# Kernel tuning notes

Measured on AMD Instinct MI355X. Metric: run time of the kernel, lower is better.

The kernel has to match this reference:

```python
import jax, jax.numpy as jnp
import numpy as np

N = 50000          # nodes
E = 1_600_000      # edges (avg degree 32)
H = 2              # attention heads per layer
F = 64             # per-head feature dim
NC = 16            # num_classes
NEG_SLOPE = 0.2    # PyG GATConv default leaky relu slope


def setup_inputs():
    key = jax.random.key(0)
    ks = jax.random.split(key, 20)
    s = 0.05
    z = jnp.zeros
    inp = {
        'x': jax.random.normal(ks[0], (N, 64), dtype=jnp.float32),
        'edge_index': jax.random.randint(ks[1], (2, E), 0, N, dtype=jnp.int32),
        # GAT layer 1: in=64 (heads=1 concat from input), out=H*F
        'W1': jax.random.normal(ks[2], (64, H * F)) * s,
        'a_src1': jax.random.normal(ks[3], (H, F)) * s,
        'a_dst1': jax.random.normal(ks[4], (H, F)) * s,
        'b1': z((H * F,)),
        # GAT layer 2: in=H*F=128, out=H*F
        'W2': jax.random.normal(ks[5], (H * F, H * F)) * s,
        'a_src2': jax.random.normal(ks[6], (H, F)) * s,
        'a_dst2': jax.random.normal(ks[7], (H, F)) * s,
        'b2': z((H * F,)),
        # MLP head: 128 -> 512 -> 256 -> NC
        'lw1': jax.random.normal(ks[8], (H * F, 512)) * s, 'lb1': z((512,)),
        'lw2': jax.random.normal(ks[9], (512, 256)) * s, 'lb2': z((256,)),
        'lw3': jax.random.normal(ks[10], (256, NC)) * s, 'lb3': z((NC,)),
    }
    return inp


def gat_conv(x, src, dst, W, a_src, a_dst, b):
    """PyG-style GATConv (shared weights for src/dst), head concat output."""
    h = (x @ W).reshape(-1, H, F)                       # [N, H, F]
    alpha_s = jnp.einsum('nhf,hf->nh', h, a_src)        # [N, H]
    alpha_d = jnp.einsum('nhf,hf->nh', h, a_dst)
    e = jax.nn.leaky_relu(alpha_s[src] + alpha_d[dst], NEG_SLOPE)  # [E', H]
    # segment softmax over incoming edges of each dst node
    e_max = jax.ops.segment_max(e, dst, num_segments=N)            # [N, H]
    e_exp = jnp.exp(e - e_max[dst])
    denom = jax.ops.segment_sum(e_exp, dst, num_segments=N)
    alpha = e_exp / (denom[dst] + 1e-16)                            # [E', H]
    msg = h[src] * alpha[:, :, None]                                # [E', H, F]
    out = jax.ops.segment_sum(msg, dst, num_segments=N)             # [N, H, F]
    return out.reshape(N, H * F) + b


def reference(x, edge_index, W1, a_src1, a_dst1, b1, W2, a_src2, a_dst2, b2,
              lw1, lb1, lw2, lb2, lw3, lb3):
    # add self loops (PyG GATConv default)
    loop = jnp.arange(N, dtype=edge_index.dtype)
    src = jnp.concatenate([edge_index[0], loop])
    dst = jnp.concatenate([edge_index[1], loop])

    h = jax.nn.relu(gat_conv(x, src, dst, W1, a_src1, a_dst1, b1))
    emb = jax.nn.relu(gat_conv(h, src, dst, W2, a_src2, a_dst2, b2))

    z = jax.nn.relu(emb @ lw1 + lb1)
    z = jax.nn.relu(z @ lw2 + lb2)
    logits = z @ lw3 + lb3
    return emb, logits
```

## Files before the change

kernel.cpp:

```cpp
#include <hip/hip_runtime.h>

typedef __bf16 bf16f __attribute__((ext_vector_type(8)));
typedef float  f32x4 __attribute__((ext_vector_type(4)));

__device__ __forceinline__ float bf2f(unsigned short u) {
  union { unsigned int u; float f; } v;
  v.u = ((unsigned int)u) << 16;
  return v.f;
}
__device__ __forceinline__ unsigned short f2bf(float f) {
  union { float f; unsigned int u; } v; v.f = f;
  unsigned int r = v.u + 0x7FFFu + ((v.u >> 16) & 1u);
  return (unsigned short)(r >> 16);
}
__device__ __forceinline__ float bflo(unsigned int w) {
  union { unsigned int u; float f; } v; v.u = w << 16; return v.f;
}
__device__ __forceinline__ float bfhi(unsigned int w) {
  union { unsigned int u; float f; } v; v.u = w & 0xFFFF0000u; return v.f;
}

__global__ void GNNModel_general_12077448036407_kernel(int* cnt, int ncnt) {
  int i = blockIdx.x * blockDim.x + threadIdx.x;
  if (i < ncnt) cnt[i] = 0;
}

__global__ void wpack2_kernel(const float* __restrict__ lw1, unsigned short* __restrict__ Wb1,
                              const float* __restrict__ lw2, unsigned short* __restrict__ Wb2) {
  int i = blockIdx.x * blockDim.x + threadIdx.x;
  if (i < 512 * 128) {
    int n = i >> 7, k = i & 127;
    Wb1[i] = f2bf(lw1[(size_t)k * 512 + n]);
  }
  if (i < 256 * 512) {
    int n = i >> 9, k = i & 511;
    Wb2[i] = f2bf(lw2[(size_t)k * 256 + n]);
  }
}

__launch_bounds__(256)
__global__ void gr_fused_kernel(const float* __restrict__ x, const float* __restrict__ W1,
                                unsigned short* __restrict__ hb, int M, int gblocks,
                                const int* __restrict__ dst, int* __restrict__ cnt,
                                unsigned short* __restrict__ rank, int E) {
  __shared__ float As[16][132];
  __shared__ float Bs[16][136];
  int bid = blockIdx.x;
  int t = threadIdx.x;

  if (bid >= gblocks) {
    int e = (bid - gblocks) * 256 + t;
    if (e < E) {
      int r = atomicAdd(&cnt[dst[e]], 1);
      rank[e] = (unsigned short)r;
    }
    return;
  }

  int tx = t & 15, ty = t >> 4;
  int m0 = bid * 128;

  float acc[8][8];
#pragma unroll
  for (int i = 0; i < 8; i++)
#pragma unroll
    for (int j = 0; j < 8; j++) acc[i][j] = 0.0f;

  int arow = t >> 1;
  int akc  = (t & 1) * 8;
  int bkk  = t >> 4;
  int bnn  = (t & 15) * 8;
  int gm = m0 + arow;

  for (int k0 = 0; k0 < 64; k0 += 16) {
    float av[8];
    if (gm < M) {
      const float* Af = x + (size_t)gm * 64 + k0 + akc;
      float4 r0 = *(const float4*)Af;
      float4 r1 = *(const float4*)(Af + 4);
      av[0] = r0.x; av[1] = r0.y; av[2] = r0.z; av[3] = r0.w;
      av[4] = r1.x; av[5] = r1.y; av[6] = r1.z; av[7] = r1.w;
    } else {
#pragma unroll
      for (int j = 0; j < 8; j++) av[j] = 0.0f;
    }
#pragma unroll
    for (int j = 0; j < 8; j++) As[akc + j][arow] = av[j];

    const float* bp = W1 + (size_t)(k0 + bkk) * 128 + bnn;
    float4 b0 = *(const float4*)bp;
    float4 b1 = *(const float4*)(bp + 4);
    *(float4*)&Bs[bkk][bnn]     = b0;
    *(float4*)&Bs[bkk][bnn + 4] = b1;

    __syncthreads();

#pragma unroll 4
    for (int kk = 0; kk < 16; kk++) {
      float a[8], b[8];
      *(float4*)&a[0] = *(const float4*)&As[kk][ty * 8];
      *(float4*)&a[4] = *(const float4*)&As[kk][ty * 8 + 4];
      *(float4*)&b[0] = *(const float4*)&Bs[kk][tx * 8];
      *(float4*)&b[4] = *(const float4*)&Bs[kk][tx * 8 + 4];
#pragma unroll
      for (int i = 0; i < 8; i++)
#pragma unroll
        for (int j = 0; j < 8; j++)
          acc[i][j] = fmaf(a[i], b[j], acc[i][j]);
    }
    __syncthreads();
  }

#pragma unroll
  for (int i = 0; i < 8; i++) {
    int m = m0 + ty * 8 + i;
    if (m >= M) continue;
    unsigned short* Cp = hb + (size_t)m * 128 + tx * 8;
    uint4 pk;
    pk.x = (unsigned int)f2bf(acc[i][0]) | ((unsigned int)f2bf(acc[i][1]) << 16);
    pk.y = (unsigned int)f2bf(acc[i][2]) | ((unsigned int)f2bf(acc[i][3]) << 16);
    pk.z = (unsigned int)f2bf(acc[i][4]) | ((unsigned int)f2bf(acc[i][5]) << 16);
    pk.w = (unsigned int)f2bf(acc[i][6]) | ((unsigned int)f2bf(acc[i][7]) << 16);
    *(uint4*)Cp = pk;
  }
}

__global__ void scan1_kernel(const int* __restrict__ cnt, int* __restrict__ offs,
                             int* __restrict__ bsum, int M) {
  __shared__ int sh[256];
  int t = threadIdx.x;
  int i = blockIdx.x * 256 + t;
  int v = (i < M) ? cnt[i] : 0;
  sh[t] = v;
  __syncthreads();
  for (int off = 1; off < 256; off <<= 1) {
    int u = (t >= off) ? sh[t - off] : 0;
    __syncthreads();
    sh[t] += u;
    __syncthreads();
  }
  if (i <= M) offs[i] = sh[t] - v;
  if (t == 255) bsum[blockIdx.x] = sh[255];
}

__global__ void scan2_kernel(int* __restrict__ bsum, int NB) {
  __shared__ int sh[256];
  int t = threadIdx.x;
  int v = (t < NB) ? bsum[t] : 0;
  sh[t] = v;
  __syncthreads();
  for (int off = 1; off < 256; off <<= 1) {
    int u = (t >= off) ? sh[t - off] : 0;
    __syncthreads();
    sh[t] += u;
    __syncthreads();
  }
  if (t < NB) bsum[t] = sh[t] - v;
}

__global__ void scan3_kernel(int* __restrict__ offs, const int* __restrict__ bsum, int M) {
  int i = blockIdx.x * 256 + threadIdx.x;
  if (i <= M) offs[i] += bsum[i >> 8];
}

__global__ void pa_fused_kernel(const unsigned short* __restrict__ hb,
                                const float* __restrict__ a_src,
                                const float* __restrict__ a_dst,
                                float2* __restrict__ aSp, float2* __restrict__ aDp,
                                int M, int ablocks,
                                const int* __restrict__ src, const int* __restrict__ dstp,
                                const unsigned short* __restrict__ rank,
                                const int* __restrict__ offs, int* __restrict__ csr, int E) {
  int bid = blockIdx.x;
  int t = threadIdx.x;

  if (bid >= ablocks) {
    int e = (bid - ablocks) * 256 + t;
    if (e < E) {
      int p = offs[dstp[e]] + (int)rank[e];
      __builtin_nontemporal_store(src[e], &csr[p]);
    }
    return;
  }

  int gw = (bid * 256 + t) >> 6;
  int lane = t & 63;
  if (gw >= M) return;
  float h0 = bf2f(hb[(size_t)gw * 128 + lane]);
  float h1 = bf2f(hb[(size_t)gw * 128 + 64 + lane]);
  float as0 = h0 * a_src[lane];
  float as1 = h1 * a_src[64 + lane];
  float ad0 = h0 * a_dst[lane];
  float ad1 = h1 * a_dst[64 + lane];
  for (int o = 32; o; o >>= 1) {
    as0 += __shfl_xor(as0, o);
    as1 += __shfl_xor(as1, o);
    ad0 += __shfl_xor(ad0, o);
    ad1 += __shfl_xor(ad1, o);
  }
  if (lane == 0) {
    aSp[gw] = make_float2(as0, as1);
    aDp[gw] = make_float2(ad0, ad1);
  }
}

__launch_bounds__(256)
__global__ void m128_kernel(const void* __restrict__ A,
                            const unsigned short* __restrict__ Bw,
                            const float* __restrict__ bias, void* __restrict__ C,
                            int M, int K, int Nt, int aBF, int cBF, int relu) {
  __shared__ unsigned short As[128 * 32];
  __shared__ unsigned short Bs[128 * 32];
  int tid = threadIdx.x;
  int wid = tid >> 6, lane = tid & 63;
  int lm = lane & 15, quad = lane >> 4;
  int wr = wid >> 1, wc = wid & 1;
  int n0 = blockIdx.x * 128, m0 = blockIdx.y * 128;

  f32x4 acc[4][4];
#pragma unroll
  for (int mi = 0; mi < 4; mi++)
#pragma unroll
    for (int ni = 0; ni < 4; ni++)
#pragma unroll
      for (int i = 0; i < 4; i++) acc[mi][ni][i] = 0.0f;

  int c0 = (wid << 6) + lane;
  int c1 = c0 + 256;
  int srow = tid >> 1;
  int skc  = (tid & 1) << 4;

  for (int k0 = 0; k0 < K; k0 += 32) {
    {
      const unsigned short* g0 = Bw + (size_t)(n0 + (c0 >> 2)) * K + k0 + ((c0 & 3) << 3);
      __builtin_amdgcn_global_load_lds((const __attribute__((address_space(1))) void*)g0,
                                       (__attribute__((address_space(3))) void*)(Bs + (wid << 9)),
                                       16, 0, 0);
      const unsigned short* g1 = Bw + (size_t)(n0 + (c1 >> 2)) * K + k0 + ((c1 & 3) << 3);
      __builtin_amdgcn_global_load_lds((const __attribute__((address_space(1))) void*)g1,
                                       (__attribute__((address_space(3))) void*)(Bs + 2048 + (wid << 9)),
                                       16, 0, 0);
    }
    if (aBF) {
      int r0 = m0 + (c0 >> 2); if (r0 > M - 1) r0 = M - 1;
      const unsigned short* g0 = (const unsigned short*)A + (size_t)r0 * K + k0 + ((c0 & 3) << 3);
      __builtin_amdgcn_global_load_lds((const __attribute__((address_space(1))) void*)g0,
                                       (__attribute__((address_space(3))) void*)(As + (wid << 9)),
                                       16, 0, 0);
      int r1 = m0 + (c1 >> 2); if (r1 > M - 1) r1 = M - 1;
      const unsigned short* g1 = (const unsigned short*)A + (size_t)r1 * K + k0 + ((c1 & 3) << 3);
      __builtin_amdgcn_global_load_lds((const __attribute__((address_space(1))) void*)g1,
                                       (__attribute__((address_space(3))) void*)(As + 2048 + (wid << 9)),
                                       16, 0, 0);
    } else {
      int gm = m0 + srow;
      uint4 p0, p1;
      if (gm < M) {
        const float* Af = (const float*)A + (size_t)gm * K + k0 + skc;
        float4 r0 = *(const float4*)Af;
        float4 r1 = *(const float4*)(Af + 4);
        float4 r2 = *(const float4*)(Af + 8);
        float4 r3 = *(const float4*)(Af + 12);
        p0.x = (unsigned int)f2bf(r0.x) | ((unsigned int)f2bf(r0.y) << 16);
        p0.y = (unsigned int)f2bf(r0.z) | ((unsigned int)f2bf(r0.w) << 16);
        p0.z = (unsigned int)f2bf(r1.x) | ((unsigned int)f2bf(r1.y) << 16);
        p0.w = (unsigned int)f2bf(r1.z) | ((unsigned int)f2bf(r1.w) << 16);
        p1.x = (unsigned int)f2bf(r2.x) | ((unsigned int)f2bf(r2.y) << 16);
        p1.y = (unsigned int)f2bf(r2.z) | ((unsigned int)f2bf(r2.w) << 16);
        p1.z = (unsigned int)f2bf(r3.x) | ((unsigned int)f2bf(r3.y) << 16);
        p1.w = (unsigned int)f2bf(r3.z) | ((unsigned int)f2bf(r3.w) << 16);
      } else {
        p0.x = p0.y = p0.z = p0.w = 0u;
        p1.x = p1.y = p1.z = p1.w = 0u;
      }
      *(uint4*)&As[srow * 32 + skc] = p0;
      *(uint4*)&As[srow * 32 + skc + 8] = p1;
    }
    __syncthreads();

    bf16f afr[4], bfr[4];
#pragma unroll
    for (int mi = 0; mi < 4; mi++)
      afr[mi] = *(const bf16f*)&As[(wr * 64 + mi * 16 + lm) * 32 + quad * 8];
#pragma unroll
    for (int ni = 0; ni < 4; ni++)
      bfr[ni] = *(const bf16f*)&Bs[(wc * 64 + ni * 16 + lm) * 32 + quad * 8];
#pragma unroll
    for (int mi = 0; mi < 4; mi++)
#pragma unroll
      for (int ni = 0; ni < 4; ni++)
        acc[mi][ni] = __builtin_amdgcn_mfma_f32_16x16x32_bf16(afr[mi], bfr[ni], acc[mi][ni], 0, 0, 0);
    __syncthreads();
  }

#pragma unroll
  for (int ni = 0; ni < 4; ni++) {
    int col = n0 + wc * 64 + ni * 16 + lm;
    float bv = (bias != 0) ? bias[col] : 0.0f;
#pragma unroll
    for (int mi = 0; mi < 4; mi++) {
#pragma unroll
      for (int i = 0; i < 4; i++) {
        int row = m0 + wr * 64 + mi * 16 + quad * 4 + i;
        if (row < M) {
          float v = acc[mi][ni][i] + bv;
          if (relu) v = fmaxf(v, 0.0f);
          if (cBF) ((unsigned short*)C)[(size_t)row * Nt + col] = f2bf(v);
          else     ((float*)C)[(size_t)row * Nt + col] = v;
        }
      }
    }
  }
}

__launch_bounds__(256)
__global__ void lgemm_kernel(const unsigned short* __restrict__ A,
                             const float* __restrict__ W,
                             const float* __restrict__ bias, float* __restrict__ C,
                             int M, int K) {
  __shared__ unsigned short Bt[16 * 264];
  int tid = threadIdx.x;
  int wave = tid >> 6, lane = tid & 63;
  int lm = lane & 15, quad = lane >> 4;
  int m0 = blockIdx.x * 64;

  for (int f0 = tid * 4; f0 < K * 16; f0 += 1024) {
    float4 w4 = *(const float4*)(W + f0);
    int k = f0 >> 4, n = f0 & 15;
    Bt[(n + 0) * 264 + k] = f2bf(w4.x);
    Bt[(n + 1) * 264 + k] = f2bf(w4.y);
    Bt[(n + 2) * 264 + k] = f2bf(w4.z);
    Bt[(n + 3) * 264 + k] = f2bf(w4.w);
  }
  __syncthreads();

  f32x4 acc;
#pragma unroll
  for (int i = 0; i < 4; i++) acc[i] = 0.0f;

  int m = m0 + wave * 16 + lm;
  const unsigned short* Ap = A + (size_t)m * K;

  for (int k0 = 0; k0 < K; k0 += 32) {
    bf16f af;
#pragma unroll
    for (int j = 0; j < 8; j++) af[j] = (__bf16)0.0f;
    if (m < M) af = *(const bf16f*)(Ap + k0 + quad * 8);
    bf16f bfv = *(const bf16f*)&Bt[lm * 264 + k0 + quad * 8];
    acc = __builtin_amdgcn_mfma_f32_16x16x32_bf16(af, bfv, acc, 0, 0, 0);
  }

  float bv = bias[lm];
#pragma unroll
  for (int i = 0; i < 4; i++) {
    int row = m0 + wave * 16 + quad * 4 + i;
    if (row < M) C[(size_t)row * 16 + lm] = acc[i] + bv;
  }
}

__launch_bounds__(256)
__global__ void tgemm_kernel(const void* __restrict__ A, const float* __restrict__ W,
                             const float* __restrict__ bias, void* __restrict__ C,
                             int M, int K, int Nt, int aBF, int cBF, int relu) {
  __shared__ float As[16][132];
  __shared__ float Bs[16][136];
  int t = threadIdx.x;
  int tx = t & 15, ty = t >> 4;
  int m0 = blockIdx.x * 128, n0 = blockIdx.y * 128;

  float acc[8][8];
#pragma unroll
  for (int i = 0; i < 8; i++)
#pragma unroll
    for (int j = 0; j < 8; j++) acc[i][j] = 0.0f;

  int arow = t >> 1;
  int akc  = (t & 1) * 8;
  int bkk  = t >> 4;
  int bnn  = (t & 15) * 8;
  int gm = m0 + arow;

  for (int k0 = 0; k0 < K; k0 += 16) {
    float av[8];
    if (gm < M) {
      if (aBF) {
        const unsigned short* Ab = (const unsigned short*)A + (size_t)gm * K + k0 + akc;
        uint4 raw = *(const uint4*)Ab;
        av[0] = bflo(raw.x); av[1] = bfhi(raw.x);
        av[2] = bflo(raw.y); av[3] = bfhi(raw.y);
        av[4] = bflo(raw.z); av[5] = bfhi(raw.z);
        av[6] = bflo(raw.w); av[7] = bfhi(raw.w);
      } else {
        const float* Af = (const float*)A + (size_t)gm * K + k0 + akc;
        float4 r0 = *(const float4*)Af;
        float4 r1 = *(const float4*)(Af + 4);
        av[0] = r0.x; av[1] = r0.y; av[2] = r0.z; av[3] = r0.w;
        av[4] = r1.x; av[5] = r1.y; av[6] = r1.z; av[7] = r1.w;
      }
    } else {
#pragma unroll
      for (int j = 0; j < 8; j++) av[j] = 0.0f;
    }
#pragma unroll
    for (int j = 0; j < 8; j++) As[akc + j][arow] = av[j];

    const float* bp = W + (size_t)(k0 + bkk) * Nt + n0 + bnn;
    float4 b0 = *(const float4*)bp;
    float4 b1 = *(const float4*)(bp + 4);
    *(float4*)&Bs[bkk][bnn]     = b0;
    *(float4*)&Bs[bkk][bnn + 4] = b1;

    __syncthreads();

#pragma unroll 4
    for (int kk = 0; kk < 16; kk++) {
      float a[8], b[8];
      *(float4*)&a[0] = *(const float4*)&As[kk][ty * 8];
      *(float4*)&a[4] = *(const float4*)&As[kk][ty * 8 + 4];
      *(float4*)&b[0] = *(const float4*)&Bs[kk][tx * 8];
      *(float4*)&b[4] = *(const float4*)&Bs[kk][tx * 8 + 4];
#pragma unroll
      for (int i = 0; i < 8; i++)
#pragma unroll
        for (int j = 0; j < 8; j++)
          acc[i][j] = fmaf(a[i], b[j], acc[i][j]);
    }
    __syncthreads();
  }

  float bv[8];
#pragma unroll
  for (int j = 0; j < 8; j++) bv[j] = (bias != 0) ? bias[n0 + tx * 8 + j] : 0.0f;

#pragma unroll
  for (int i = 0; i < 8; i++) {
    int m = m0 + ty * 8 + i;
    if (m >= M) continue;
    float v[8];
#pragma unroll
    for (int j = 0; j < 8; j++) {
      float s = acc[i][j] + bv[j];
      v[j] = relu ? fmaxf(s, 0.0f) : s;
    }
    if (cBF) {
      unsigned short* Cp = (unsigned short*)C + (size_t)m * Nt + n0 + tx * 8;
      uint4 pk;
      pk.x = (unsigned int)f2bf(v[0]) | ((unsigned int)f2bf(v[1]) << 16);
      pk.y = (unsigned int)f2bf(v[2]) | ((unsigned int)f2bf(v[3]) << 16);
      pk.z = (unsigned int)f2bf(v[4]) | ((unsigned int)f2bf(v[5]) << 16);
      pk.w = (unsigned int)f2bf(v[6]) | ((unsigned int)f2bf(v[7]) << 16);
      *(uint4*)Cp = pk;
    } else {
      float* Cp = (float*)C + (size_t)m * Nt + n0 + tx * 8;
      float4 o0; o0.x = v[0]; o0.y = v[1]; o0.z = v[2]; o0.w = v[3];
      float4 o1; o1.x = v[4]; o1.y = v[5]; o1.z = v[6]; o1.w = v[7];
      *(float4*)Cp = o0;
      *(float4*)(Cp + 4) = o1;
    }
  }
}

__global__ void alphas_kernel(const unsigned short* __restrict__ hb,
                              const float* __restrict__ a_src,
                              const float* __restrict__ a_dst,
                              float2* __restrict__ aSp, float2* __restrict__ aDp, int M) {
  int gw = (blockIdx.x * blockDim.x + threadIdx.x) >> 6;
  int lane = threadIdx.x & 63;
  if (gw >= M) return;
  float h0 = bf2f(hb[(size_t)gw * 128 + lane]);
  float h1 = bf2f(hb[(size_t)gw * 128 + 64 + lane]);
  float as0 = h0 * a_src[lane];
  float as1 = h1 * a_src[64 + lane];
  float ad0 = h0 * a_dst[lane];
  float ad1 = h1 * a_dst[64 + lane];
  for (int o = 32; o; o >>= 1) {
    as0 += __shfl_xor(as0, o);
    as1 += __shfl_xor(as1, o);
    ad0 += __shfl_xor(ad0, o);
    ad1 += __shfl_xor(ad1, o);
  }
  if (lane == 0) {
    aSp[gw] = make_float2(as0, as1);
    aDp[gw] = make_float2(ad0, ad1);
  }
}

__global__ void aggregate_kernel(const unsigned short* __restrict__ hb,
                                 const float2* __restrict__ aSp,
                                 const float2* __restrict__ aDp,
                                 const int* __restrict__ csr_src, const int* __restrict__ offs,
                                 const float* __restrict__ bias,
                                 float* __restrict__ out, int M) {
  int n = (blockIdx.x * blockDim.x + threadIdx.x) >> 6;
  int lane = threadIdx.x & 63;
  if (n >= M) return;
  int g = lane >> 4;
  int q = lane & 15;
  int h0sel = (q < 8);

  float2 adn = aDp[n];
  float2 asn = aSp[n];
  float e0 = asn.x + adn.x; e0 = (e0 > 0.0f) ? e0 : 0.2f * e0;
  float e1 = asn.y + adn.y; e1 = (e1 > 0.0f) ? e1 : 0.2f * e1;
  float ws0 = expf(e0), ws1 = expf(e1);
  float wself = h0sel ? ws0 : ws1;

  float acc[8];
  if (g == 0) {
    uint4 rv = *(const uint4*)(hb + (size_t)n * 128 + q * 8);
    acc[0] = wself * bflo(rv.x); acc[1] = wself * bfhi(rv.x);
    acc[2] = wself * bflo(rv.y); acc[3] = wself * bfhi(rv.y);
    acc[4] = wself * bflo(rv.z); acc[5] = wself * bfhi(rv.z);
    acc[6] = wself * bflo(rv.w); acc[7] = wself * bfhi(rv.w);
  } else {
#pragma unroll
    for (int i = 0; i < 8; i++) acc[i] = 0.0f;
  }

  float lp0 = 0.0f, lp1 = 0.0f;
  int rs = offs[n], re = offs[n + 1];
  for (int base = rs; base < re; base += 64) {
    int cnt = re - base; if (cnt > 64) cnt = 64;
    int s = 0; float w0 = 0.0f, w1 = 0.0f;
    if (lane < cnt) {
      s = csr_src[base + lane];
      float2 a = aSp[s];
      float f0 = a.x + adn.x; f0 = (f0 > 0.0f) ? f0 : 0.2f * f0;
      float f1 = a.y + adn.y; f1 = (f1 > 0.0f) ? f1 : 0.2f * f1;
      w0 = expf(f0); w1 = expf(f1);
      lp0 += w0; lp1 += w1;
    }
    int jmax = (cnt + 3) >> 2;
#pragma unroll 2
    for (int j = 0; j < jmax; j++) {
      int el = 4 * j + g;
      int sj  = __shfl(s, el);
      float w0j = __shfl(w0, el);
      float w1j = __shfl(w1, el);
      float wj = h0sel ? w0j : w1j;
      uint4 rv = *(const uint4*)(hb + (size_t)sj * 128 + q * 8);
      acc[0] = fmaf(wj, bflo(rv.x), acc[0]);
      acc[1] = fmaf(wj, bfhi(rv.x), acc[1]);
      acc[2] = fmaf(wj, bflo(rv.y), acc[2]);
      acc[3] = fmaf(wj, bfhi(rv.y), acc[3]);
      acc[4] = fmaf(wj, bflo(rv.z), acc[4]);
      acc[5] = fmaf(wj, bfhi(rv.z), acc[5]);
      acc[6] = fmaf(wj, bflo(rv.w), acc[6]);
      acc[7] = fmaf(wj, bfhi(rv.w), acc[7]);
    }
  }
#pragma unroll
  for (int i = 0; i < 8; i++) {
    acc[i] += __shfl_xor(acc[i], 16);
    acc[i] += __shfl_xor(acc[i], 32);
  }
  for (int o = 32; o; o >>= 1) {
    lp0 += __shfl_xor(lp0, o);
    lp1 += __shfl_xor(lp1, o);
  }
  if (g == 0) {
    float linv = 1.0f / ((h0sel ? lp0 + ws0 : lp1 + ws1) + 1e-16f);
    const float* bp = bias + q * 8;
    float4 o0, o1;
    o0.x = fmaxf(acc[0] * linv + bp[0], 0.0f);
    o0.y = fmaxf(acc[1] * linv + bp[1], 0.0f);
    o0.z = fmaxf(acc[2] * linv + bp[2], 0.0f);
    o0.w = fmaxf(acc[3] * linv + bp[3], 0.0f);
    o1.x = fmaxf(acc[4] * linv + bp[4], 0.0f);
    o1.y = fmaxf(acc[5] * linv + bp[5], 0.0f);
    o1.z = fmaxf(acc[6] * linv + bp[6], 0.0f);
    o1.w = fmaxf(acc[7] * linv + bp[7], 0.0f);
    float* op = out + (size_t)n * 128 + q * 8;
    *(float4*)op = o0;
    *(float4*)(op + 4) = o1;
  }
}

extern "C" void kernel_launch(void* const* d_in, const int* in_sizes, int n_in,
                              void* d_out, int out_size, void* d_ws, size_t ws_size,
                              hipStream_t stream) {
  const int N = in_sizes[0] / 64;
  const int E = in_sizes[1] / 2;
  const float* x   = (const float*)d_in[0];
  const int*   ei  = (const int*)d_in[1];
  const float* W1  = (const float*)d_in[2];
  const float* as1 = (const float*)d_in[3];
  const float* ad1 = (const float*)d_in[4];
  const float* b1  = (const float*)d_in[5];
  const float* W2  = (const float*)d_in[6];
  const float* as2 = (const float*)d_in[7];
  const float* ad2 = (const float*)d_in[8];
  const float* b2  = (const float*)d_in[9];
  const float* lw1 = (const float*)d_in[10];
  const float* lb1 = (const float*)d_in[11];
  const float* lw2 = (const float*)d_in[12];
  const float* lb2 = (const float*)d_in[13];
  const float* lw3 = (const float*)d_in[14];
  const float* lb3 = (const float*)d_in[15];

  float* emb    = (float*)d_out;
  float* logits = (float*)d_out + (size_t)N * 128;

  char* base = (char*)d_ws;
  size_t o = 0;
  unsigned short* Wb1 = (unsigned short*)(base + o); o += ((size_t)512 * 128 * 2 + 255) & ~(size_t)255;
  unsigned short* Wb2 = (unsigned short*)(base + o); o += ((size_t)256 * 512 * 2 + 255) & ~(size_t)255;
  char* tb = base + o;

  size_t t = 0;
  unsigned short* hb = (unsigned short*)(tb + t); t += ((size_t)N * 128 * 2 + 255) & ~(size_t)255;
  float* x2f = (float*)(tb + t); t += ((size_t)N * 128 * 4 + 255) & ~(size_t)255;
  float2* aSp = (float2*)(tb + t); t += ((size_t)N * 8 + 255) & ~(size_t)255;
  float2* aDp = (float2*)(tb + t); t += ((size_t)N * 8 + 255) & ~(size_t)255;
  int* cnt  = (int*)(tb + t); t += ((size_t)N * 4 + 255) & ~(size_t)255;
  int* offs = (int*)(tb + t); t += ((size_t)(N + 1) * 4 + 255) & ~(size_t)255;
  int* bsum = (int*)(tb + t); t += ((size_t)256 * 4 + 255) & ~(size_t)255;
  unsigned short* rank = (unsigned short*)(tb + t); t += ((size_t)E * 2 + 255) & ~(size_t)255;
  int* csr  = (int*)(tb + t); t += ((size_t)E * 4 + 255) & ~(size_t)255;
  unsigned short* z1b = (unsigned short*)tb;
  unsigned short* z2b = (unsigned short*)(tb + (((size_t)N * 512 * 2 + 255) & ~(size_t)255));

  const int* esrc = ei;
  const int* edst = ei + E;

  int eb = (E + 255) / 256;
  int sb = (N + 256) / 256;
  int nb4 = (N + 3) / 4;
  int mtb = (N + 127) / 128;

  GNNModel_general_12077448036407_kernel<<<(N + 255) / 256, 256, 0, stream>>>(cnt, N);
  wpack2_kernel<<<512, 256, 0, stream>>>(lw1, Wb1, lw2, Wb2);

  gr_fused_kernel<<<mtb + eb, 256, 0, stream>>>(x, W1, hb, N, mtb, edst, cnt, rank, E);

  scan1_kernel<<<sb, 256, 0, stream>>>(cnt, offs, bsum, N);
  scan2_kernel<<<1, 256, 0, stream>>>(bsum, sb);
  scan3_kernel<<<sb, 256, 0, stream>>>(offs, bsum, N);

  pa_fused_kernel<<<nb4 + eb, 256, 0, stream>>>(hb, as1, ad1, aSp, aDp, N, nb4,
                                                esrc, edst, rank, offs, csr, E);

  aggregate_kernel<<<nb4, 256, 0, stream>>>(hb, aSp, aDp, csr, offs, b1, x2f, N);

  tgemm_kernel<<<dim3(mtb, 1), 256, 0, stream>>>(x2f, W2, (const float*)0, hb,
                                                 N, 128, 128, 0, 1, 0);
  alphas_kernel<<<nb4, 256, 0, stream>>>(hb, as2, ad2, aSp, aDp, N);
  aggregate_kernel<<<nb4, 256, 0, stream>>>(hb, aSp, aDp, csr, offs, b2, emb, N);

  m128_kernel<<<dim3(4, mtb), 256, 0, stream>>>(emb, Wb1, lb1, z1b,
                                                N, 128, 512, 0, 1, 1);
  m128_kernel<<<dim3(2, mtb), 256, 0, stream>>>(z1b, Wb2, lb2, z2b,
                                                N, 512, 256, 1, 1, 1);
  int mtb64 = (N + 63) / 64;
  lgemm_kernel<<<mtb64, 256, 0, stream>>>(z2b, lw3, lb3, logits, N, 256);
}
```

Before: 503.5 us.

## Remap MLP GEMM tiles per XCD and stage bf16 epilogue through LDS

```diff
diff --git a/kernel.cpp b/kernel.cpp
--- a/kernel.cpp
+++ b/kernel.cpp
@@ -208,14 +208,25 @@
 __global__ void m128_kernel(const void* __restrict__ A,
                             const unsigned short* __restrict__ Bw,
                             const float* __restrict__ bias, void* __restrict__ C,
-                            int M, int K, int Nt, int aBF, int cBF, int relu) {
-  __shared__ unsigned short As[128 * 32];
-  __shared__ unsigned short Bs[128 * 32];
+                            int M, int K, int Nt, int aBF, int cBF, int relu,
+                            int mtiles, int lgNB) {
+  __shared__ unsigned short sh[8704];
+  unsigned short* As = sh;
+  unsigned short* Bs = sh + 4096;
   int tid = threadIdx.x;
   int wid = tid >> 6, lane = tid & 63;
   int lm = lane & 15, quad = lane >> 4;
   int wr = wid >> 1, wc = wid & 1;
-  int n0 = blockIdx.x * 128, m0 = blockIdx.y * 128;
+
+  int xcd = blockIdx.x;
+  int slot = blockIdx.y;
+  int qm = mtiles >> 3, rm = mtiles & 7;
+  int cntm = qm + (xcd < rm);
+  int mstart = xcd * qm + (xcd < rm ? xcd : rm);
+  if (slot >= (cntm << lgNB)) return;
+  int NBm1 = (1 << lgNB) - 1;
+  int m0 = (mstart + (slot >> lgNB)) * 128;
+  int n0 = (slot & NBm1) * 128;
 
   f32x4 acc[4][4];
 #pragma unroll
@@ -293,20 +304,54 @@
     __syncthreads();
   }
 
-#pragma unroll
-  for (int ni = 0; ni < 4; ni++) {
-    int col = n0 + wc * 64 + ni * 16 + lm;
-    float bv = (bias != 0) ? bias[col] : 0.0f;
-#pragma unroll
-    for (int mi = 0; mi < 4; mi++) {
-#pragma unroll
-      for (int i = 0; i < 4; i++) {
-        int row = m0 + wr * 64 + mi * 16 + quad * 4 + i;
-        if (row < M) {
-          float v = acc[mi][ni][i] + bv;
-          if (relu) v = fmaxf(v, 0.0f);
-          if (cBF) ((unsigned short*)C)[(size_t)row * Nt + col] = f2bf(v);
-          else     ((float*)C)[(size_t)row * Nt + col] = v;
+  if (cBF) {
+#pragma unroll
+    for (int p = 0; p < 2; p++) {
+      __syncthreads();
+      if (wc == p) {
+#pragma unroll
+        for (int ni = 0; ni < 4; ni++) {
+          int colb = ni * 16 + lm;
+          float bv = (bias != 0) ? bias[n0 + p * 64 + colb] : 0.0f;
+#pragma unroll
+          for (int mi = 0; mi < 4; mi++) {
+#pragma unroll
+            for (int i = 0; i < 4; i++) {
+              int rowb = wr * 64 + mi * 16 + quad * 4 + i;
+              float v = acc[mi][ni][i] + bv;
+              if (relu) v = fmaxf(v, 0.0f);
+              sh[rowb * 68 + colb] = f2bf(v);
+            }
+          }
+        }
+      }
+      __syncthreads();
+#pragma unroll
+      for (int sweep = 0; sweep < 4; sweep++) {
+        int rowb = (tid >> 3) + 32 * sweep;
+        int seg = tid & 7;
+        int grow = m0 + rowb;
+        if (grow < M) {
+          uint4 val = *(const uint4*)&sh[rowb * 68 + seg * 8];
+          *(uint4*)((unsigned short*)C + (size_t)grow * Nt + n0 + p * 64 + seg * 8) = val;
+        }
+      }
+    }
+  } else {
+#pragma unroll
+    for (int ni = 0; ni < 4; ni++) {
+      int col = n0 + wc * 64 + ni * 16 + lm;
+      float bv = (bias != 0) ? bias[col] : 0.0f;
+#pragma unroll
+      for (int mi = 0; mi < 4; mi++) {
+#pragma unroll
+        for (int i = 0; i < 4; i++) {
+          int row = m0 + wr * 64 + mi * 16 + quad * 4 + i;
+          if (row < M) {
+            float v = acc[mi][ni][i] + bv;
+            if (relu) v = fmaxf(v, 0.0f);
+            ((float*)C)[(size_t)row * Nt + col] = v;
+          }
         }
       }
     }
@@ -647,10 +692,12 @@
   alphas_kernel<<<nb4, 256, 0, stream>>>(hb, as2, ad2, aSp, aDp, N);
   aggregate_kernel<<<nb4, 256, 0, stream>>>(hb, aSp, aDp, csr, offs, b2, emb, N);
 
-  m128_kernel<<<dim3(4, mtb), 256, 0, stream>>>(emb, Wb1, lb1, z1b,
-                                                N, 128, 512, 0, 1, 1);
-  m128_kernel<<<dim3(2, mtb), 256, 0, stream>>>(z1b, Wb2, lb2, z2b,
-                                                N, 512, 256, 1, 1, 1);
+  int qx = mtb >> 3, rx = mtb & 7;
+  int spx = qx + (rx ? 1 : 0);
+  m128_kernel<<<dim3(8, spx * 4), 256, 0, stream>>>(emb, Wb1, lb1, z1b,
+                                                    N, 128, 512, 0, 1, 1, mtb, 2);
+  m128_kernel<<<dim3(8, spx * 2), 256, 0, stream>>>(z1b, Wb2, lb2, z2b,
+                                                    N, 512, 256, 1, 1, 1, mtb, 1);
   int mtb64 = (N + 63) / 64;
   lgemm_kernel<<<mtb64, 256, 0, stream>>>(z2b, lw3, lb3, logits, N, 256);
 }
```

After: 467.6 us. 1.08x faster.
